# Performance work log

Hardware: AMD Instinct MI355X
Metric: run time of the kernel (lower is better)

Reference implementation:

```python
import jax, jax.numpy as jnp
import numpy as np

# Static config (matches init_kwargs)
N = 1024        # node_num
F = 64          # input_dim (window length)
D = 64          # dim == embed_dim (heads=1)
TOPK = 20
B = 64
EPS = 1e-5      # BatchNorm eps
NEG_SLOPE = 0.2 # GraphLayer leaky_relu slope


def setup_inputs() -> dict:
    key = jax.random.key(0)
    ks = jax.random.split(key, 12)
    s = lambda fan: 1.0 / np.sqrt(fan)
    inp = {
        'data': jax.random.normal(ks[0], (B, N, F), jnp.float32),
        'org_edge_index': jax.random.randint(ks[1], (2, 2048), 0, N),
        'embedding': jax.random.normal(ks[2], (N, D), jnp.float32) * s(D),   # nn.Embedding(node_num, dim), xavier-ish
        'lin_w': jax.random.normal(ks[3], (F, D), jnp.float32) * s(F),       # GraphLayer lin (bias=False)
        'att_i': jax.random.normal(ks[4], (D,), jnp.float32) * s(D),
        'att_j': jax.random.normal(ks[5], (D,), jnp.float32) * s(D),
        'att_em_i': jax.random.normal(ks[6], (D,), jnp.float32) * s(D),
        'att_em_j': jax.random.normal(ks[7], (D,), jnp.float32) * s(D),
        'gnn_bias': jnp.zeros((D,), jnp.float32),
        'bn1_gamma': jnp.ones((D,), jnp.float32),  # GNNLayer.bn
        'bn1_beta': jnp.zeros((D,), jnp.float32),
        'bn2_gamma': jnp.ones((D,), jnp.float32),  # bn_outlayer_in
        'bn2_beta': jnp.zeros((D,), jnp.float32),
        'out_w': jax.random.normal(ks[8], (D, 1), jnp.float32) * s(D),       # OutLayer Linear(dim, 1)
        'out_b': jnp.zeros((1,), jnp.float32),
    }
    return inp


def _batchnorm(x, gamma, beta, axes):
    # training-mode BatchNorm: batch statistics over `axes`, per-feature affine
    mu = jnp.mean(x, axis=axes, keepdims=True)
    var = jnp.var(x, axis=axes, keepdims=True)
    return gamma * (x - mu) * jax.lax.rsqrt(var + EPS) + beta


def reference(data, org_edge_index, embedding, lin_w, att_i, att_j, att_em_i,
              att_em_j, gnn_bias, bn1_gamma, bn1_beta, bn2_gamma, bn2_beta,
              out_w, out_b):
    # --- dynamic graph construction from embedding cosine similarity ---
    w = jax.lax.stop_gradient(embedding)          # weights_arr.detach()
    nrm = jnp.linalg.norm(w, axis=-1)
    cos = (w @ w.T) / jnp.clip(nrm[:, None] * nrm[None, :], 1e-10)
    _, topi = jax.lax.top_k(cos, TOPK)            # [N, TOPK] neighbors j of each target i
    # (torch code drops edges whose cos value is exactly 0 -- measure-zero with
    #  random embeddings; edge count stays N*TOPK. Self edge i->i is always in topk,
    #  matching remove_self_loops + add_self_loops.)

    # --- GraphLayer (GAT-style, heads=1, concat=False, aggr='add') ---
    xl = jnp.einsum('bnf,fd->bnd', data, lin_w)   # linear transform, [B,N,D]
    xj = xl[:, topi]                               # gather neighbor feats [B,N,TOPK,D]
    ej = embedding[topi]                           # neighbor embeddings [N,TOPK,D]
    # alpha = <key_i, att_i||att_em_i> + <key_j, att_j||att_em_j>
    score = (xl @ att_i)[:, :, None] \
          + (embedding @ att_em_i)[None, :, None] \
          + jnp.einsum('bnkd,d->bnk', xj, att_j) \
          + (ej @ att_em_j)[None]                  # [B,N,TOPK]
    alpha = jax.nn.softmax(jax.nn.leaky_relu(score, NEG_SLOPE), axis=-1)
    gnn = jnp.einsum('bnk,bnkd->bnd', alpha, xj) + gnn_bias

    # GNNLayer.bn: BatchNorm1d over B*N samples, D channels
    gnn = _batchnorm(gnn, bn1_gamma, bn1_beta, axes=(0, 1))

    # --- readout ---
    out = gnn * embedding[None]                    # mul with node embedding
    out = jax.nn.relu(_batchnorm(out, bn2_gamma, bn2_beta, axes=(0, 1)))
    # dropout(0.2) -> identity (eval)
    pred = (out @ out_w + out_b).reshape(B, N)     # OutLayer: Linear(D, 1)
    return pred, out
```

## Files before the change

### kernel.cpp

```cpp
#include <hip/hip_runtime.h>

#define NN 1024
#define KK 20
#define BN 65536
#define NEG_SLOPE 0.2f

typedef unsigned short u16;
typedef unsigned int u32;
typedef unsigned long long u64;
typedef __attribute__((ext_vector_type(8))) short bf8;
typedef __attribute__((ext_vector_type(4))) float f32x4;

__device__ __forceinline__ float bf2f(u16 h) {
    return __uint_as_float(((u32)h) << 16);
}
__device__ __forceinline__ u16 f2bf(float f) {
    u32 u = __float_as_uint(f);
    u32 lsb = (u >> 16) & 1u;
    u += 0x7fffu + lsb;
    return (u16)(u >> 16);
}
__device__ __forceinline__ void up2(u32 w, float& a, float& b) {
    a = __uint_as_float(w << 16);
    b = __uint_as_float(w & 0xffff0000u);
}
__device__ __forceinline__ bool is_bf(const void* g1) {
    return *(const u32*)g1 == 0x3F803F80u;
}
template <bool BF>
__device__ __forceinline__ float ldf(const void* p, size_t i) {
    if (BF) return bf2f(((const u16*)p)[i]);
    return ((const float*)p)[i];
}
template <bool BF>
__device__ __forceinline__ void stf(void* p, size_t i, float v) {
    if (BF) ((u16*)p)[i] = f2bf(v);
    else ((float*)p)[i] = v;
}
template <bool BF>
__device__ __forceinline__ void ldf2(const void* p, size_t pairidx, float& a, float& b) {
    if (BF) {
        u32 w = ((const u32*)p)[pairidx];
        up2(w, a, b);
    } else {
        float2 v = ((const float2*)p)[pairidx];
        a = v.x;
        b = v.y;
    }
}
__device__ __forceinline__ void gl2lds16(const void* g, void* l) {
    __builtin_amdgcn_global_load_lds(
        (const __attribute__((address_space(1))) u32*)g,
        (__attribute__((address_space(3))) u32*)l, 16, 0, 0);
}
__device__ __forceinline__ float ldstat(const float* p) {
    return __hip_atomic_load(p, __ATOMIC_RELAXED, __HIP_MEMORY_SCOPE_AGENT);
}

template <bool BF>
__device__ void k1a_body(const void* emb, const void* aei, const void* aej,
                         u16* nwH, u16* nwL, float* e_i, float* e_j, float* stats) {
    int tid = threadIdx.x;
    if (blockIdx.x == 0) {
        for (int s = tid; s < 464; s += 256) stats[s] = 0.f;
    }
    int lane = tid & 63, wave = tid >> 6;
    int n = blockIdx.x * 4 + wave;
    float v = ldf<BF>(emb, n * 64 + lane);
    float s2 = v * v;
    float si = v * ldf<BF>(aei, lane);
    float sj = v * ldf<BF>(aej, lane);
#pragma unroll
    for (int off = 32; off; off >>= 1) {
        s2 += __shfl_xor(s2, off, 64);
        si += __shfl_xor(si, off, 64);
        sj += __shfl_xor(sj, off, 64);
    }
    float rq = rsqrtf(fmaxf(s2, 1e-20f));
    float x = v * rq;
    u16 h = f2bf(x);
    nwH[n * 64 + lane] = h;
    nwL[n * 64 + lane] = f2bf(x - bf2f(h));
    if (lane == 0) { e_i[n] = si; e_j[n] = sj; }
}
__global__ __launch_bounds__(256) void k1a_norm(const void* emb, const void* aei, const void* aej,
                                                const void* probe, u16* nwH, u16* nwL,
                                                float* e_i, float* e_j, float* stats) {
    if (is_bf(probe)) k1a_body<true>(emb, aei, aej, nwH, nwL, e_i, e_j, stats);
    else k1a_body<false>(emb, aei, aej, nwH, nwL, e_i, e_j, stats);
}

__global__ __launch_bounds__(256) void k1b_gram(const u16* __restrict__ nwH,
                                                const u16* __restrict__ nwL,
                                                float* __restrict__ G) {
    int tid = threadIdx.x;
    int lane = tid & 63, wave = tid >> 6;
    int c = lane & 15, quad = lane >> 4;
    int rowblk = blockIdx.x >> 4, colblk = blockIdx.x & 15;
    int arow = rowblk * 64 + wave * 16 + c;
    bf8 aH[2], aL[2];
#pragma unroll
    for (int s = 0; s < 2; ++s) {
        aH[s] = *(const bf8*)(nwH + (size_t)arow * 64 + s * 32 + quad * 8);
        aL[s] = *(const bf8*)(nwL + (size_t)arow * 64 + s * 32 + quad * 8);
    }
    f32x4 acc[4] = {{0.f, 0.f, 0.f, 0.f}, {0.f, 0.f, 0.f, 0.f}, {0.f, 0.f, 0.f, 0.f}, {0.f, 0.f, 0.f, 0.f}};
#pragma unroll
    for (int t = 0; t < 4; ++t) {
        int bnode = colblk * 64 + t * 16 + c;
#pragma unroll
        for (int s = 0; s < 2; ++s) {
            bf8 bH = *(const bf8*)(nwH + (size_t)bnode * 64 + s * 32 + quad * 8);
            bf8 bL = *(const bf8*)(nwL + (size_t)bnode * 64 + s * 32 + quad * 8);
            acc[t] = __builtin_amdgcn_mfma_f32_16x16x32_bf16(aH[s], bH, acc[t], 0, 0, 0);
            acc[t] = __builtin_amdgcn_mfma_f32_16x16x32_bf16(aH[s], bL, acc[t], 0, 0, 0);
            acc[t] = __builtin_amdgcn_mfma_f32_16x16x32_bf16(aL[s], bH, acc[t], 0, 0, 0);
        }
    }
#pragma unroll
    for (int t = 0; t < 4; ++t) {
#pragma unroll
        for (int reg = 0; reg < 4; ++reg) {
            int row = rowblk * 64 + wave * 16 + quad * 4 + reg;
            G[(size_t)row * 1024 + colblk * 64 + t * 16 + c] = acc[t][reg];
        }
    }
}

__device__ void k1c_body(int blk, const float* __restrict__ G, int* __restrict__ topi) {
    int lane = threadIdx.x & 63, wave = threadIdx.x >> 6;
    int n = blk * 4 + wave;
    const f32x4* gp = (const f32x4*)(G + (size_t)n * 1024 + lane * 16);
    f32x4 v0 = gp[0], v1 = gp[1], v2 = gp[2], v3 = gp[3];
    float c[16] = {v0.x, v0.y, v0.z, v0.w, v1.x, v1.y, v1.z, v1.w,
                   v2.x, v2.y, v2.z, v2.w, v3.x, v3.y, v3.z, v3.w};
    u32 o[16];
#pragma unroll
    for (int j = 0; j < 16; ++j) {
        u32 u = __float_as_uint(c[j]);
        o[j] = u ^ (u32)(((int)u >> 31) | 0x80000000);
    }
    unsigned mask = 0u;
    int keep = 0;
    for (int r = 0; r < KK; ++r) {
        u32 bo = 0u;
        int bj = 0;
#pragma unroll
        for (int j = 0; j < 16; ++j) {
            bool t = !((mask >> j) & 1u) && o[j] > bo;
            bo = t ? o[j] : bo;
            bj = t ? j : bj;
        }
        u64 key = ((u64)bo << 32) | (u32)(~(u32)(lane * 16 + bj));
#pragma unroll
        for (int off = 32; off; off >>= 1) {
            u64 ok = __shfl_xor((unsigned long long)key, off, 64);
            key = ok > key ? ok : key;
        }
        int bm = (int)((~(u32)key) & 1023u);
        if ((bm >> 4) == lane) mask |= 1u << (bm & 15);
        if (lane == r) keep = bm;
    }
    if (lane < KK) topi[n * KK + lane] = keep;
}

template <bool BF>
__device__ void k2_body(int blk, const void* data, const void* lin_w, const void* att_i,
                        const void* att_j, u16* xl, float* a_i, float* a_j) {
    __shared__ u16 Bl[64 * 72];
    __shared__ u16 Ct[64 * 72];
    int tid = threadIdx.x;
    {
        int k = tid >> 2, n0 = (tid & 3) * 16;
        if (BF) {
            const u16* lw = (const u16*)lin_w;
#pragma unroll
            for (int i = 0; i < 16; ++i) Bl[(n0 + i) * 72 + k] = lw[k * 64 + n0 + i];
        } else {
            const float* lw = (const float*)lin_w;
#pragma unroll
            for (int i = 0; i < 16; ++i) Bl[(n0 + i) * 72 + k] = f2bf(lw[k * 64 + n0 + i]);
        }
    }
    __syncthreads();
    int lane = tid & 63, wave = tid >> 6;
    int c = lane & 15, quad = lane >> 4;
    int m0 = blk * 64 + wave * 16;
    size_t row = (size_t)(m0 + c);
    f32x4 acc[4] = {{0.f, 0.f, 0.f, 0.f}, {0.f, 0.f, 0.f, 0.f}, {0.f, 0.f, 0.f, 0.f}, {0.f, 0.f, 0.f, 0.f}};
#pragma unroll
    for (int s = 0; s < 2; ++s) {
        bf8 a;
        if (BF) {
            a = *(const bf8*)((const u16*)data + row * 64 + s * 32 + quad * 8);
        } else {
            const float* dp = (const float*)data + row * 64 + s * 32 + quad * 8;
            f32x4 x0 = *(const f32x4*)dp;
            f32x4 x1 = *(const f32x4*)(dp + 4);
            a[0] = (short)f2bf(x0.x); a[1] = (short)f2bf(x0.y);
            a[2] = (short)f2bf(x0.z); a[3] = (short)f2bf(x0.w);
            a[4] = (short)f2bf(x1.x); a[5] = (short)f2bf(x1.y);
            a[6] = (short)f2bf(x1.z); a[7] = (short)f2bf(x1.w);
        }
#pragma unroll
        for (int t = 0; t < 4; ++t) {
            bf8 b = *(const bf8*)&Bl[(t * 16 + c) * 72 + s * 32 + quad * 8];
            acc[t] = __builtin_amdgcn_mfma_f32_16x16x32_bf16(a, b, acc[t], 0, 0, 0);
        }
    }
    float wi[4], wj[4];
#pragma unroll
    for (int t = 0; t < 4; ++t) {
        wi[t] = ldf<BF>(att_i, t * 16 + c);
        wj[t] = ldf<BF>(att_j, t * 16 + c);
    }
    float ai4[4] = {0.f, 0.f, 0.f, 0.f}, aj4[4] = {0.f, 0.f, 0.f, 0.f};
#pragma unroll
    for (int t = 0; t < 4; ++t) {
#pragma unroll
        for (int reg = 0; reg < 4; ++reg) {
            float v = acc[t][reg];
            Ct[(wave * 16 + quad * 4 + reg) * 72 + t * 16 + c] = f2bf(v);
            ai4[reg] += v * wi[t];
            aj4[reg] += v * wj[t];
        }
    }
#pragma unroll
    for (int reg = 0; reg < 4; ++reg) {
#pragma unroll
        for (int off = 1; off < 16; off <<= 1) {
            ai4[reg] += __shfl_xor(ai4[reg], off, 64);
            aj4[reg] += __shfl_xor(aj4[reg], off, 64);
        }
    }
    if (c == 0) {
#pragma unroll
        for (int reg = 0; reg < 4; ++reg) {
            a_i[m0 + quad * 4 + reg] = ai4[reg];
            a_j[m0 + quad * 4 + reg] = aj4[reg];
        }
    }
    __syncthreads();
    {
        int r = tid >> 2, seg = tid & 3;
        uint4 v0 = *(const uint4*)&Ct[r * 72 + seg * 16];
        uint4 v1 = *(const uint4*)&Ct[r * 72 + seg * 16 + 8];
        uint4* dst = (uint4*)xl + ((size_t)(blk * 64 + r) * 8 + seg * 2);
        dst[0] = v0;
        dst[1] = v1;
    }
}

__global__ __launch_bounds__(256) void k12_fused(const void* data, const void* lin_w,
                                                 const void* att_i, const void* att_j,
                                                 const void* probe, u16* xl, float* a_i,
                                                 float* a_j, const float* G, int* topi) {
    if (blockIdx.x < 1024) {
        if (is_bf(probe)) k2_body<true>(blockIdx.x, data, lin_w, att_i, att_j, xl, a_i, a_j);
        else k2_body<false>(blockIdx.x, data, lin_w, att_i, att_j, xl, a_i, a_j);
    } else {
        k1c_body(blockIdx.x - 1024, G, topi);
    }
}

template <bool BF>
__device__ __forceinline__ void pqr_for(const float* stats, const void* g1, const void* b1,
                                        const void* g2, const void* b2, int d,
                                        float& P, float& Q, float& R) {
    double inv = 1.0 / 65536.0;
    double S1 = ldstat(stats + d), S2 = ldstat(stats + 64 + d);
    double T1 = ldstat(stats + 128 + d), T2 = ldstat(stats + 192 + d);
    double T3 = ldstat(stats + 256 + d), U1 = ldstat(stats + 320 + d), U2 = ldstat(stats + 384 + d);
    double mu1 = S1 * inv;
    double var1 = S2 * inv - mu1 * mu1;
    if (var1 < 0.0) var1 = 0.0;
    double r1 = 1.0 / sqrt(var1 + 1e-5);
    double A = (double)ldf<BF>(g1, d) * r1;
    double C = (double)ldf<BF>(b1, d) - A * mu1;
    double E1 = A * T1 + C * U1;
    double mu2 = E1 * inv;
    double E2 = A * A * T2 + 2.0 * A * C * T3 + C * C * U2;
    double var2 = E2 * inv - mu2 * mu2;
    if (var2 < 0.0) var2 = 0.0;
    double r2 = 1.0 / sqrt(var2 + 1e-5);
    double g2r2 = (double)ldf<BF>(g2, d) * r2;
    P = (float)(g2r2 * A);
    Q = (float)(g2r2 * C);
    R = (float)((double)ldf<BF>(b2, d) - g2r2 * mu2);
}
template <bool BF>
__device__ void k35_body(const u16* xl, const int* topi, const float* a_i, const float* a_j,
                         const float* e_i, const float* e_j, const void* emb,
                         const void* gnn_bias, const void* g1, const void* b1,
                         const void* g2, const void* b2, const void* out_w, const void* out_b,
                         float* stats, int* ctr, void* dout) {
    extern __shared__ char smem[];
    u32* slice = (u32*)smem;
    float* aje = (float*)(smem + 131072);
    float* aie = (float*)(smem + 135168);
    u32* sp = (u32*)(smem + 136192);
    int tid = threadIdx.x;
    int b = blockIdx.x & 63;
    int q = blockIdx.x >> 6;
    int n0 = q * 256;
    int lane = tid & 63, wave = tid >> 6;
    const char* srcb = (const char*)xl + (((size_t)b) << 17);
#pragma unroll
    for (int r = 0; r < 8; ++r) {
        int off = r * 16384 + wave * 1024;
        gl2lds16(srcb + off + lane * 16, (char*)smem + off);
    }
    aje[tid] = a_j[(b << 10) + tid] + e_j[tid];
    if (tid < 256) aie[tid] = a_i[(b << 10) + n0 + tid] + e_i[n0 + tid];
    __syncthreads();
    int half = lane >> 5, hl = lane & 31;
    int hwid = wave * 2 + half;
    int nl0 = hwid * 8;
#pragma unroll 2
    for (int ii = 0; ii < 8; ++ii) {
        int nl = nl0 + ii;
        int t = (hl < KK) ? topi[(n0 + nl) * KK + hl] : 0;
        float sc = -3e38f;
        if (hl < KK) {
            sc = aie[nl] + aje[t];
            sc = sc >= 0.f ? sc : NEG_SLOPE * sc;
        }
        float m = sc;
#pragma unroll
        for (int off = 16; off; off >>= 1) m = fmaxf(m, __shfl_xor(m, off, 32));
        float p = (hl < KK) ? __expf(sc - m) : 0.f;
        float S = p;
#pragma unroll
        for (int off = 16; off; off >>= 1) S += __shfl_xor(S, off, 32);
        if (hl < KK) sp[(hwid * 8 + ii) * KK + hl] = ((u32)f2bf(p / S) << 16) | (u32)t;
    }
    float bias0, bias1;
    ldf2<BF>(gnn_bias, hl, bias0, bias1);
    float se[14];
#pragma unroll
    for (int s = 0; s < 14; ++s) se[s] = 0.f;
    u32 gv[8];
#pragma unroll
    for (int ii = 0; ii < 8; ++ii) {
        int nl = nl0 + ii;
        int n = n0 + nl;
        const u32* spp = &sp[(hwid * 8 + ii) * KK];
        float a0e = 0.f, a0o = 0.f, a1e = 0.f, a1o = 0.f;
#pragma unroll
        for (int k = 0; k < KK; k += 2) {
            uint2 vv = *(const uint2*)&spp[k];
            u32 w0 = slice[((vv.x & 1023u) << 5) + hl];
            u32 w1 = slice[((vv.y & 1023u) << 5) + hl];
            float p0 = __uint_as_float(vv.x & 0xffff0000u);
            float p1 = __uint_as_float(vv.y & 0xffff0000u);
            a0e += p0 * __uint_as_float(w0 << 16);
            a1e += p0 * __uint_as_float(w0 & 0xffff0000u);
            a0o += p1 * __uint_as_float(w1 << 16);
            a1o += p1 * __uint_as_float(w1 & 0xffff0000u);
        }
        float acc0 = a0e + a0o + bias0;
        float acc1 = a1e + a1o + bias1;
        gv[ii] = (u32)f2bf(acc0) | ((u32)f2bf(acc1) << 16);
        float em0, em1;
        ldf2<BF>(emb, n * 32 + hl, em0, em1);
        se[0] += acc0; se[1] += acc1;
        se[2] += acc0 * acc0; se[3] += acc1 * acc1;
        float ge0 = acc0 * em0, ge1 = acc1 * em1;
        se[4] += ge0; se[5] += ge1;
        se[6] += ge0 * ge0; se[7] += ge1 * ge1;
        se[8] += ge0 * em0; se[9] += ge1 * em1;
        se[10] += em0; se[11] += em1;
        se[12] += em0 * em0; se[13] += em1 * em1;
    }
#pragma unroll
    for (int s = 0; s < 14; ++s) se[s] += __shfl_xor(se[s], 32, 64);
    __syncthreads();
    float* ps = (float*)smem;
    if (half == 0) {
#pragma unroll
        for (int s = 0; s < 7; ++s) {
            ps[wave * 448 + s * 64 + 2 * hl] = se[2 * s];
            ps[wave * 448 + s * 64 + 2 * hl + 1] = se[2 * s + 1];
        }
    }
    __syncthreads();
    if (tid < 448) {
        float s = 0.f;
#pragma unroll
        for (int w = 0; w < 16; ++w) s += ps[w * 448 + tid];
        atomicAdd(&stats[tid], s);
    }
    __syncthreads();
    if (tid == 0) {
        __hip_atomic_fetch_add(ctr, 1, __ATOMIC_ACQ_REL, __HIP_MEMORY_SCOPE_AGENT);
        while (__hip_atomic_load(ctr, __ATOMIC_ACQUIRE, __HIP_MEMORY_SCOPE_AGENT) < 256) {
            __builtin_amdgcn_s_sleep(8);
        }
    }
    __syncthreads();
    float P0, Q0, R0, P1, Q1, R1;
    pqr_for<BF>(stats, g1, b1, g2, b2, 2 * hl, P0, Q0, R0);
    pqr_for<BF>(stats, g1, b1, g2, b2, 2 * hl + 1, P1, Q1, R1);
    float wo0, wo1;
    ldf2<BF>(out_w, hl, wo0, wo1);
    float ob = ldf<BF>(out_b, 0);
#pragma unroll
    for (int ii = 0; ii < 8; ++ii) {
        int n = n0 + nl0 + ii;
        int pair = (b << 10) + n;
        float g0, g1v;
        up2(gv[ii], g0, g1v);
        float em0, em1;
        ldf2<BF>(emb, n * 32 + hl, em0, em1);
        float o0 = fmaxf(P0 * g0 * em0 + Q0 * em0 + R0, 0.f);
        float o1 = fmaxf(P1 * g1v * em1 + Q1 * em1 + R1, 0.f);
        if (BF) {
            ((u32*)dout)[(BN >> 1) + pair * 32 + hl] = (u32)f2bf(o0) | ((u32)f2bf(o1) << 16);
        } else {
            float2 v2; v2.x = o0; v2.y = o1;
            ((float2*)dout)[(BN >> 1) + pair * 32 + hl] = v2;
        }
        float p = o0 * wo0 + o1 * wo1;
#pragma unroll
        for (int off = 16; off; off >>= 1) p += __shfl_xor(p, off, 32);
        if (hl == 0) stf<BF>(dout, pair, p + ob);
    }
}
__global__ __launch_bounds__(1024) void k35_gnn(const u16* xl, const int* topi, const float* a_i,
                                                const float* a_j, const float* e_i, const float* e_j,
                                                const void* emb, const void* gnn_bias,
                                                const void* g1, const void* b1, const void* g2,
                                                const void* b2, const void* out_w, const void* out_b,
                                                float* stats, int* ctr, void* dout) {
    if (is_bf(g1)) k35_body<true>(xl, topi, a_i, a_j, e_i, e_j, emb, gnn_bias, g1, b1, g2, b2,
                                  out_w, out_b, stats, ctr, dout);
    else k35_body<false>(xl, topi, a_i, a_j, e_i, e_j, emb, gnn_bias, g1, b1, g2, b2,
                         out_w, out_b, stats, ctr, dout);
}

extern "C" void kernel_launch(void* const* d_in, const int* in_sizes, int n_in,
                              void* d_out, int out_size, void* d_ws, size_t ws_size,
                              hipStream_t stream) {
    const void* data = d_in[0];
    const void* emb = d_in[2];
    const void* lin_w = d_in[3];
    const void* att_i = d_in[4];
    const void* att_j = d_in[5];
    const void* att_em_i = d_in[6];
    const void* att_em_j = d_in[7];
    const void* gnn_bias = d_in[8];
    const void* bn1_g = d_in[9];
    const void* bn1_b = d_in[10];
    const void* bn2_g = d_in[11];
    const void* bn2_b = d_in[12];
    const void* out_w = d_in[13];
    const void* out_b = d_in[14];

    char* ws = (char*)d_ws;
    float* a_i = (float*)ws;
    float* a_j = a_i + 65536;
    float* e_i = a_j + 65536;
    float* e_j = e_i + 1024;
    float* stats = e_j + 1024;
    int* ctr = (int*)(stats + 448);
    int* topi = (int*)(stats + 464);
    u16* xl = (u16*)(topi + 20480);
    u16* nwH = xl + 4194304;
    u16* nwL = nwH + 65536;
    float* G = (float*)(nwL + 65536);

    k1a_norm<<<256, 256, 0, stream>>>(emb, att_em_i, att_em_j, bn1_g, nwH, nwL, e_i, e_j, stats);
    k1b_gram<<<256, 256, 0, stream>>>(nwH, nwL, G);
    k12_fused<<<1280, 256, 0, stream>>>(data, lin_w, att_i, att_j, bn1_g, xl, a_i, a_j, G, topi);
    k35_gnn<<<256, 1024, 156672, stream>>>(xl, topi, a_i, a_j, e_i, e_j, emb, gnn_bias,
                                           bn1_g, bn1_b, bn2_g, bn2_b, out_w, out_b,
                                           stats, ctr, d_out);
}
```

Measured before the change: 157.3 us.

## Gather neighbor features from global memory and split GNN kernel into smaller blocks

```diff
diff --git a/kernel.cpp b/kernel.cpp
--- a/kernel.cpp
+++ b/kernel.cpp
@@ -48,11 +48,6 @@
         b = v.y;
     }
 }
-__device__ __forceinline__ void gl2lds16(const void* g, void* l) {
-    __builtin_amdgcn_global_load_lds(
-        (const __attribute__((address_space(1))) u32*)g,
-        (__attribute__((address_space(3))) u32*)l, 16, 0, 0);
-}
 __device__ __forceinline__ float ldstat(const float* p) {
     return __hip_atomic_load(p, __ATOMIC_RELAXED, __HIP_MEMORY_SCOPE_AGENT);
 }
@@ -62,7 +57,7 @@
                          u16* nwH, u16* nwL, float* e_i, float* e_j, float* stats) {
     int tid = threadIdx.x;
     if (blockIdx.x == 0) {
-        for (int s = tid; s < 464; s += 256) stats[s] = 0.f;
+        for (int s = tid; s < 1808; s += 256) stats[s] = 0.f;
     }
     int lane = tid & 63, wave = tid >> 6;
     int n = blockIdx.x * 4 + wave;
@@ -264,13 +259,15 @@
 }
 
 template <bool BF>
-__device__ __forceinline__ void pqr_for(const float* stats, const void* g1, const void* b1,
+__device__ __forceinline__ void pqr_lds(const float* sc, const void* g1, const void* b1,
                                         const void* g2, const void* b2, int d,
                                         float& P, float& Q, float& R) {
     double inv = 1.0 / 65536.0;
-    double S1 = ldstat(stats + d), S2 = ldstat(stats + 64 + d);
-    double T1 = ldstat(stats + 128 + d), T2 = ldstat(stats + 192 + d);
-    double T3 = ldstat(stats + 256 + d), U1 = ldstat(stats + 320 + d), U2 = ldstat(stats + 384 + d);
+#define SUM4(off) ((double)sc[(off) + d] + (double)sc[448 + (off) + d] + \
+                   (double)sc[896 + (off) + d] + (double)sc[1344 + (off) + d])
+    double S1 = SUM4(0), S2 = SUM4(64), T1 = SUM4(128), T2 = SUM4(192);
+    double T3 = SUM4(256), U1 = SUM4(320), U2 = SUM4(384);
+#undef SUM4
     double mu1 = S1 * inv;
     double var1 = S2 * inv - mu1 * mu1;
     if (var1 < 0.0) var1 = 0.0;
@@ -289,33 +286,28 @@
     R = (float)((double)ldf<BF>(b2, d) - g2r2 * mu2);
 }
 template <bool BF>
-__device__ void k35_body(const u16* xl, const int* topi, const float* a_i, const float* a_j,
+__device__ void k3g_body(const u16* xl, const int* topi, const float* a_i, const float* a_j,
                          const float* e_i, const float* e_j, const void* emb,
                          const void* gnn_bias, const void* g1, const void* b1,
                          const void* g2, const void* b2, const void* out_w, const void* out_b,
                          float* stats, int* ctr, void* dout) {
-    extern __shared__ char smem[];
-    u32* slice = (u32*)smem;
-    float* aje = (float*)(smem + 131072);
-    float* aie = (float*)(smem + 135168);
-    u32* sp = (u32*)(smem + 136192);
+    __shared__ float aje[1024];
+    __shared__ float aie[128];
+    __shared__ u32 sp[16 * 8 * KK];
+    __shared__ float ps[8 * 448];
     int tid = threadIdx.x;
-    int b = blockIdx.x & 63;
-    int q = blockIdx.x >> 6;
-    int n0 = q * 256;
+    int bid = blockIdx.x;
+    int b = bid & 63;
+    int j = bid >> 6;
+    int n0 = j * 128;
     int lane = tid & 63, wave = tid >> 6;
-    const char* srcb = (const char*)xl + (((size_t)b) << 17);
-#pragma unroll
-    for (int r = 0; r < 8; ++r) {
-        int off = r * 16384 + wave * 1024;
-        gl2lds16(srcb + off + lane * 16, (char*)smem + off);
-    }
-    aje[tid] = a_j[(b << 10) + tid] + e_j[tid];
-    if (tid < 256) aie[tid] = a_i[(b << 10) + n0 + tid] + e_i[n0 + tid];
-    __syncthreads();
     int half = lane >> 5, hl = lane & 31;
     int hwid = wave * 2 + half;
     int nl0 = hwid * 8;
+    aje[tid] = a_j[(b << 10) + tid] + e_j[tid];
+    aje[tid + 512] = a_j[(b << 10) + tid + 512] + e_j[tid + 512];
+    if (tid < 128) aie[tid] = a_i[(b << 10) + n0 + tid] + e_i[n0 + tid];
+    __syncthreads();
 #pragma unroll 2
     for (int ii = 0; ii < 8; ++ii) {
         int nl = nl0 + ii;
@@ -340,6 +332,8 @@
 #pragma unroll
     for (int s = 0; s < 14; ++s) se[s] = 0.f;
     u32 gv[8];
+    const u32* __restrict__ xg = (const u32*)xl + ((size_t)b << 15);
+    __syncthreads();
 #pragma unroll
     for (int ii = 0; ii < 8; ++ii) {
         int nl = nl0 + ii;
@@ -349,8 +343,8 @@
 #pragma unroll
         for (int k = 0; k < KK; k += 2) {
             uint2 vv = *(const uint2*)&spp[k];
-            u32 w0 = slice[((vv.x & 1023u) << 5) + hl];
-            u32 w1 = slice[((vv.y & 1023u) << 5) + hl];
+            u32 w0 = xg[((vv.x & 1023u) << 5) + hl];
+            u32 w1 = xg[((vv.y & 1023u) << 5) + hl];
             float p0 = __uint_as_float(vv.x & 0xffff0000u);
             float p1 = __uint_as_float(vv.y & 0xffff0000u);
             a0e += p0 * __uint_as_float(w0 << 16);
@@ -375,7 +369,6 @@
 #pragma unroll
     for (int s = 0; s < 14; ++s) se[s] += __shfl_xor(se[s], 32, 64);
     __syncthreads();
-    float* ps = (float*)smem;
     if (half == 0) {
 #pragma unroll
         for (int s = 0; s < 7; ++s) {
@@ -387,20 +380,22 @@
     if (tid < 448) {
         float s = 0.f;
 #pragma unroll
-        for (int w = 0; w < 16; ++w) s += ps[w * 448 + tid];
-        atomicAdd(&stats[tid], s);
+        for (int w = 0; w < 8; ++w) s += ps[w * 448 + tid];
+        atomicAdd(&stats[(b & 3) * 448 + tid], s);
     }
     __syncthreads();
     if (tid == 0) {
         __hip_atomic_fetch_add(ctr, 1, __ATOMIC_ACQ_REL, __HIP_MEMORY_SCOPE_AGENT);
-        while (__hip_atomic_load(ctr, __ATOMIC_ACQUIRE, __HIP_MEMORY_SCOPE_AGENT) < 256) {
+        while (__hip_atomic_load(ctr, __ATOMIC_ACQUIRE, __HIP_MEMORY_SCOPE_AGENT) < 512) {
             __builtin_amdgcn_s_sleep(8);
         }
     }
     __syncthreads();
+    for (int s = tid; s < 1792; s += 512) ps[s] = ldstat(stats + s);
+    __syncthreads();
     float P0, Q0, R0, P1, Q1, R1;
-    pqr_for<BF>(stats, g1, b1, g2, b2, 2 * hl, P0, Q0, R0);
-    pqr_for<BF>(stats, g1, b1, g2, b2, 2 * hl + 1, P1, Q1, R1);
+    pqr_lds<BF>(ps, g1, b1, g2, b2, 2 * hl, P0, Q0, R0);
+    pqr_lds<BF>(ps, g1, b1, g2, b2, 2 * hl + 1, P1, Q1, R1);
     float wo0, wo1;
     ldf2<BF>(out_w, hl, wo0, wo1);
     float ob = ldf<BF>(out_b, 0);
@@ -426,15 +421,15 @@
         if (hl == 0) stf<BF>(dout, pair, p + ob);
     }
 }
-__global__ __launch_bounds__(1024) void k35_gnn(const u16* xl, const int* topi, const float* a_i,
-                                                const float* a_j, const float* e_i, const float* e_j,
-                                                const void* emb, const void* gnn_bias,
-                                                const void* g1, const void* b1, const void* g2,
-                                                const void* b2, const void* out_w, const void* out_b,
-                                                float* stats, int* ctr, void* dout) {
-    if (is_bf(g1)) k35_body<true>(xl, topi, a_i, a_j, e_i, e_j, emb, gnn_bias, g1, b1, g2, b2,
+__global__ __launch_bounds__(512, 4) void k3g_gnn(const u16* xl, const int* topi, const float* a_i,
+                                                  const float* a_j, const float* e_i, const float* e_j,
+                                                  const void* emb, const void* gnn_bias,
+                                                  const void* g1, const void* b1, const void* g2,
+                                                  const void* b2, const void* out_w, const void* out_b,
+                                                  float* stats, int* ctr, void* dout) {
+    if (is_bf(g1)) k3g_body<true>(xl, topi, a_i, a_j, e_i, e_j, emb, gnn_bias, g1, b1, g2, b2,
                                   out_w, out_b, stats, ctr, dout);
-    else k35_body<false>(xl, topi, a_i, a_j, e_i, e_j, emb, gnn_bias, g1, b1, g2, b2,
+    else k3g_body<false>(xl, topi, a_i, a_j, e_i, e_j, emb, gnn_bias, g1, b1, g2, b2,
                          out_w, out_b, stats, ctr, dout);
 }
 
@@ -462,8 +457,8 @@
     float* e_i = a_j + 65536;
     float* e_j = e_i + 1024;
     float* stats = e_j + 1024;
-    int* ctr = (int*)(stats + 448);
-    int* topi = (int*)(stats + 464);
+    int* ctr = (int*)(stats + 1792);
+    int* topi = (int*)(stats + 1808);
     u16* xl = (u16*)(topi + 20480);
     u16* nwH = xl + 4194304;
     u16* nwL = nwH + 65536;
@@ -472,7 +467,7 @@
     k1a_norm<<<256, 256, 0, stream>>>(emb, att_em_i, att_em_j, bn1_g, nwH, nwL, e_i, e_j, stats);
     k1b_gram<<<256, 256, 0, stream>>>(nwH, nwL, G);
     k12_fused<<<1280, 256, 0, stream>>>(data, lin_w, att_i, att_j, bn1_g, xl, a_i, a_j, G, topi);
-    k35_gnn<<<256, 1024, 156672, stream>>>(xl, topi, a_i, a_j, e_i, e_j, emb, gnn_bias,
-                                           bn1_g, bn1_b, bn2_g, bn2_b, out_w, out_b,
-                                           stats, ctr, d_out);
-}
+    k3g_gnn<<<512, 512, 0, stream>>>(xl, topi, a_i, a_j, e_i, e_j, emb, gnn_bias,
+                                     bn1_g, bn1_b, bn2_g, bn2_b, out_w, out_b,
+                                     stats, ctr, d_out);
+}
```

New measurement: 207.5 us. 1.32x slower.

## Remap GNN kernel to 16-lane groups with 4 features per lane

Applied to the files above, without the earlier changes.

```diff
diff --git a/kernel.cpp b/kernel.cpp
--- a/kernel.cpp
+++ b/kernel.cpp
@@ -47,11 +47,6 @@
         a = v.x;
         b = v.y;
     }
-}
-__device__ __forceinline__ void gl2lds16(const void* g, void* l) {
-    __builtin_amdgcn_global_load_lds(
-        (const __attribute__((address_space(1))) u32*)g,
-        (__attribute__((address_space(3))) u32*)l, 16, 0, 0);
 }
 __device__ __forceinline__ float ldstat(const float* p) {
     return __hip_atomic_load(p, __ATOMIC_RELAXED, __HIP_MEMORY_SCOPE_AGENT);
@@ -264,13 +259,12 @@
 }
 
 template <bool BF>
-__device__ __forceinline__ void pqr_for(const float* stats, const void* g1, const void* b1,
+__device__ __forceinline__ void pqr_lds(const float* sc, const void* g1, const void* b1,
                                         const void* g2, const void* b2, int d,
                                         float& P, float& Q, float& R) {
     double inv = 1.0 / 65536.0;
-    double S1 = ldstat(stats + d), S2 = ldstat(stats + 64 + d);
-    double T1 = ldstat(stats + 128 + d), T2 = ldstat(stats + 192 + d);
-    double T3 = ldstat(stats + 256 + d), U1 = ldstat(stats + 320 + d), U2 = ldstat(stats + 384 + d);
+    double S1 = sc[d], S2 = sc[64 + d], T1 = sc[128 + d], T2 = sc[192 + d];
+    double T3 = sc[256 + d], U1 = sc[320 + d], U2 = sc[384 + d];
     double mu1 = S1 * inv;
     double var1 = S2 * inv - mu1 * mu1;
     if (var1 < 0.0) var1 = 0.0;
@@ -289,98 +283,111 @@
     R = (float)((double)ldf<BF>(b2, d) - g2r2 * mu2);
 }
 template <bool BF>
-__device__ void k35_body(const u16* xl, const int* topi, const float* a_i, const float* a_j,
-                         const float* e_i, const float* e_j, const void* emb,
-                         const void* gnn_bias, const void* g1, const void* b1,
-                         const void* g2, const void* b2, const void* out_w, const void* out_b,
-                         float* stats, int* ctr, void* dout) {
+__device__ void k35b_body(const u16* xl, const int* topi, const float* a_i, const float* a_j,
+                          const float* e_i, const float* e_j, const void* emb,
+                          const void* gnn_bias, const void* g1, const void* b1,
+                          const void* g2, const void* b2, const void* out_w, const void* out_b,
+                          float* stats, int* ctr, void* dout) {
     extern __shared__ char smem[];
     u32* slice = (u32*)smem;
     float* aje = (float*)(smem + 131072);
     float* aie = (float*)(smem + 135168);
-    u32* sp = (u32*)(smem + 136192);
+    u32* spg = (u32*)(smem + 136192);
     int tid = threadIdx.x;
     int b = blockIdx.x & 63;
     int q = blockIdx.x >> 6;
     int n0 = q * 256;
     int lane = tid & 63, wave = tid >> 6;
-    const char* srcb = (const char*)xl + (((size_t)b) << 17);
-#pragma unroll
-    for (int r = 0; r < 8; ++r) {
-        int off = r * 16384 + wave * 1024;
-        gl2lds16(srcb + off + lane * 16, (char*)smem + off);
-    }
+    const uint4* src = (const uint4*)(xl + ((size_t)b << 16));
+    uint4* dst = (uint4*)slice;
+#pragma unroll
+    for (int r = 0; r < 8; ++r) dst[r * 1024 + tid] = src[r * 1024 + tid];
     aje[tid] = a_j[(b << 10) + tid] + e_j[tid];
     if (tid < 256) aie[tid] = a_i[(b << 10) + n0 + tid] + e_i[n0 + tid];
     __syncthreads();
-    int half = lane >> 5, hl = lane & 31;
-    int hwid = wave * 2 + half;
-    int nl0 = hwid * 8;
+    int gid = tid >> 4, glane = tid & 15;
+    u32* spp = &spg[gid * 24];
+    float bias0, bias1, bias2, bias3;
+    ldf2<BF>(gnn_bias, 2 * glane, bias0, bias1);
+    ldf2<BF>(gnn_bias, 2 * glane + 1, bias2, bias3);
+    float se[28];
+#pragma unroll
+    for (int s = 0; s < 28; ++s) se[s] = 0.f;
+    u32 gvw[8];
 #pragma unroll 2
-    for (int ii = 0; ii < 8; ++ii) {
-        int nl = nl0 + ii;
-        int t = (hl < KK) ? topi[(n0 + nl) * KK + hl] : 0;
-        float sc = -3e38f;
-        if (hl < KK) {
-            sc = aie[nl] + aje[t];
-            sc = sc >= 0.f ? sc : NEG_SLOPE * sc;
-        }
-        float m = sc;
-#pragma unroll
-        for (int off = 16; off; off >>= 1) m = fmaxf(m, __shfl_xor(m, off, 32));
-        float p = (hl < KK) ? __expf(sc - m) : 0.f;
-        float S = p;
-#pragma unroll
-        for (int off = 16; off; off >>= 1) S += __shfl_xor(S, off, 32);
-        if (hl < KK) sp[(hwid * 8 + ii) * KK + hl] = ((u32)f2bf(p / S) << 16) | (u32)t;
-    }
-    float bias0, bias1;
-    ldf2<BF>(gnn_bias, hl, bias0, bias1);
-    float se[14];
-#pragma unroll
-    for (int s = 0; s < 14; ++s) se[s] = 0.f;
-    u32 gv[8];
-#pragma unroll
-    for (int ii = 0; ii < 8; ++ii) {
-        int nl = nl0 + ii;
+    for (int ii = 0; ii < 4; ++ii) {
+        int nl = gid * 4 + ii;
         int n = n0 + nl;
-        const u32* spp = &sp[(hwid * 8 + ii) * KK];
-        float a0e = 0.f, a0o = 0.f, a1e = 0.f, a1o = 0.f;
+        int ta = topi[n * KK + glane];
+        float aien = aie[nl];
+        float sa = aien + aje[ta];
+        sa = sa >= 0.f ? sa : NEG_SLOPE * sa;
+        int tb = 0;
+        float sb = -3e38f;
+        if (glane < 4) {
+            tb = topi[n * KK + 16 + glane];
+            sb = aien + aje[tb];
+            sb = sb >= 0.f ? sb : NEG_SLOPE * sb;
+        }
+        float m = fmaxf(sa, sb);
+#pragma unroll
+        for (int off = 8; off; off >>= 1) m = fmaxf(m, __shfl_xor(m, off, 64));
+        float pa = __expf(sa - m);
+        float pb = (glane < 4) ? __expf(sb - m) : 0.f;
+        float S = pa + pb;
+#pragma unroll
+        for (int off = 8; off; off >>= 1) S += __shfl_xor(S, off, 64);
+        spp[glane] = ((u32)f2bf(pa / S) << 16) | (u32)ta;
+        if (glane < 4) spp[16 + glane] = ((u32)f2bf(pb / S) << 16) | (u32)tb;
+        float a0e = 0.f, a1e = 0.f, a2e = 0.f, a3e = 0.f;
+        float a0o = 0.f, a1o = 0.f, a2o = 0.f, a3o = 0.f;
 #pragma unroll
         for (int k = 0; k < KK; k += 2) {
             uint2 vv = *(const uint2*)&spp[k];
-            u32 w0 = slice[((vv.x & 1023u) << 5) + hl];
-            u32 w1 = slice[((vv.y & 1023u) << 5) + hl];
+            uint2 w0 = *(const uint2*)&slice[(vv.x & 1023u) * 32 + 2 * glane];
+            uint2 w1 = *(const uint2*)&slice[(vv.y & 1023u) * 32 + 2 * glane];
             float p0 = __uint_as_float(vv.x & 0xffff0000u);
             float p1 = __uint_as_float(vv.y & 0xffff0000u);
-            a0e += p0 * __uint_as_float(w0 << 16);
-            a1e += p0 * __uint_as_float(w0 & 0xffff0000u);
-            a0o += p1 * __uint_as_float(w1 << 16);
-            a1o += p1 * __uint_as_float(w1 & 0xffff0000u);
+            a0e += p0 * __uint_as_float(w0.x << 16);
+            a1e += p0 * __uint_as_float(w0.x & 0xffff0000u);
+            a2e += p0 * __uint_as_float(w0.y << 16);
+            a3e += p0 * __uint_as_float(w0.y & 0xffff0000u);
+            a0o += p1 * __uint_as_float(w1.x << 16);
+            a1o += p1 * __uint_as_float(w1.x & 0xffff0000u);
+            a2o += p1 * __uint_as_float(w1.y << 16);
+            a3o += p1 * __uint_as_float(w1.y & 0xffff0000u);
         }
         float acc0 = a0e + a0o + bias0;
         float acc1 = a1e + a1o + bias1;
-        gv[ii] = (u32)f2bf(acc0) | ((u32)f2bf(acc1) << 16);
-        float em0, em1;
-        ldf2<BF>(emb, n * 32 + hl, em0, em1);
-        se[0] += acc0; se[1] += acc1;
-        se[2] += acc0 * acc0; se[3] += acc1 * acc1;
-        float ge0 = acc0 * em0, ge1 = acc1 * em1;
-        se[4] += ge0; se[5] += ge1;
-        se[6] += ge0 * ge0; se[7] += ge1 * ge1;
-        se[8] += ge0 * em0; se[9] += ge1 * em1;
-        se[10] += em0; se[11] += em1;
-        se[12] += em0 * em0; se[13] += em1 * em1;
-    }
-#pragma unroll
-    for (int s = 0; s < 14; ++s) se[s] += __shfl_xor(se[s], 32, 64);
+        float acc2 = a2e + a2o + bias2;
+        float acc3 = a3e + a3o + bias3;
+        gvw[2 * ii] = (u32)f2bf(acc0) | ((u32)f2bf(acc1) << 16);
+        gvw[2 * ii + 1] = (u32)f2bf(acc2) | ((u32)f2bf(acc3) << 16);
+        float em0, em1, em2, em3;
+        ldf2<BF>(emb, n * 32 + 2 * glane, em0, em1);
+        ldf2<BF>(emb, n * 32 + 2 * glane + 1, em2, em3);
+        float ge0 = acc0 * em0, ge1 = acc1 * em1, ge2 = acc2 * em2, ge3 = acc3 * em3;
+        se[0] += acc0; se[1] += acc1; se[2] += acc2; se[3] += acc3;
+        se[4] += acc0 * acc0; se[5] += acc1 * acc1; se[6] += acc2 * acc2; se[7] += acc3 * acc3;
+        se[8] += ge0; se[9] += ge1; se[10] += ge2; se[11] += ge3;
+        se[12] += ge0 * ge0; se[13] += ge1 * ge1; se[14] += ge2 * ge2; se[15] += ge3 * ge3;
+        se[16] += ge0 * em0; se[17] += ge1 * em1; se[18] += ge2 * em2; se[19] += ge3 * em3;
+        se[20] += em0; se[21] += em1; se[22] += em2; se[23] += em3;
+        se[24] += em0 * em0; se[25] += em1 * em1; se[26] += em2 * em2; se[27] += em3 * em3;
+    }
+#pragma unroll
+    for (int s = 0; s < 28; ++s) {
+        se[s] += __shfl_xor(se[s], 16, 64);
+        se[s] += __shfl_xor(se[s], 32, 64);
+    }
     __syncthreads();
     float* ps = (float*)smem;
-    if (half == 0) {
+    if (lane < 16) {
 #pragma unroll
         for (int s = 0; s < 7; ++s) {
-            ps[wave * 448 + s * 64 + 2 * hl] = se[2 * s];
-            ps[wave * 448 + s * 64 + 2 * hl + 1] = se[2 * s + 1];
+#pragma unroll
+            for (int c = 0; c < 4; ++c)
+                ps[wave * 448 + s * 64 + 4 * glane + c] = se[s * 4 + c];
         }
     }
     __syncthreads();
@@ -398,44 +405,60 @@
         }
     }
     __syncthreads();
-    float P0, Q0, R0, P1, Q1, R1;
-    pqr_for<BF>(stats, g1, b1, g2, b2, 2 * hl, P0, Q0, R0);
-    pqr_for<BF>(stats, g1, b1, g2, b2, 2 * hl + 1, P1, Q1, R1);
-    float wo0, wo1;
-    ldf2<BF>(out_w, hl, wo0, wo1);
+    float* sc = aje;
+    if (tid < 448) sc[tid] = ldstat(stats + tid);
+    __syncthreads();
+    float P0, Q0, R0, P1, Q1, R1, P2, Q2, R2, P3, Q3, R3;
+    pqr_lds<BF>(sc, g1, b1, g2, b2, 4 * glane, P0, Q0, R0);
+    pqr_lds<BF>(sc, g1, b1, g2, b2, 4 * glane + 1, P1, Q1, R1);
+    pqr_lds<BF>(sc, g1, b1, g2, b2, 4 * glane + 2, P2, Q2, R2);
+    pqr_lds<BF>(sc, g1, b1, g2, b2, 4 * glane + 3, P3, Q3, R3);
+    float wo0, wo1, wo2, wo3;
+    ldf2<BF>(out_w, 2 * glane, wo0, wo1);
+    ldf2<BF>(out_w, 2 * glane + 1, wo2, wo3);
     float ob = ldf<BF>(out_b, 0);
 #pragma unroll
-    for (int ii = 0; ii < 8; ++ii) {
-        int n = n0 + nl0 + ii;
+    for (int ii = 0; ii < 4; ++ii) {
+        int n = n0 + gid * 4 + ii;
         int pair = (b << 10) + n;
-        float g0, g1v;
-        up2(gv[ii], g0, g1v);
-        float em0, em1;
-        ldf2<BF>(emb, n * 32 + hl, em0, em1);
-        float o0 = fmaxf(P0 * g0 * em0 + Q0 * em0 + R0, 0.f);
-        float o1 = fmaxf(P1 * g1v * em1 + Q1 * em1 + R1, 0.f);
+        float v0, v1, v2, v3;
+        up2(gvw[2 * ii], v0, v1);
+        up2(gvw[2 * ii + 1], v2, v3);
+        float em0, em1, em2, em3;
+        ldf2<BF>(emb, n * 32 + 2 * glane, em0, em1);
+        ldf2<BF>(emb, n * 32 + 2 * glane + 1, em2, em3);
+        float o0 = fmaxf(P0 * v0 * em0 + Q0 * em0 + R0, 0.f);
+        float o1 = fmaxf(P1 * v1 * em1 + Q1 * em1 + R1, 0.f);
+        float o2 = fmaxf(P2 * v2 * em2 + Q2 * em2 + R2, 0.f);
+        float o3 = fmaxf(P3 * v3 * em3 + Q3 * em3 + R3, 0.f);
         if (BF) {
-            ((u32*)dout)[(BN >> 1) + pair * 32 + hl] = (u32)f2bf(o0) | ((u32)f2bf(o1) << 16);
+            uint2 ov;
+            ov.x = (u32)f2bf(o0) | ((u32)f2bf(o1) << 16);
+            ov.y = (u32)f2bf(o2) | ((u32)f2bf(o3) << 16);
+            *(uint2*)&((u32*)dout)[(BN >> 1) + pair * 32 + 2 * glane] = ov;
         } else {
-            float2 v2; v2.x = o0; v2.y = o1;
-            ((float2*)dout)[(BN >> 1) + pair * 32 + hl] = v2;
-        }
-        float p = o0 * wo0 + o1 * wo1;
-#pragma unroll
-        for (int off = 16; off; off >>= 1) p += __shfl_xor(p, off, 32);
-        if (hl == 0) stf<BF>(dout, pair, p + ob);
-    }
-}
-__global__ __launch_bounds__(1024) void k35_gnn(const u16* xl, const int* topi, const float* a_i,
-                                                const float* a_j, const float* e_i, const float* e_j,
-                                                const void* emb, const void* gnn_bias,
-                                                const void* g1, const void* b1, const void* g2,
-                                                const void* b2, const void* out_w, const void* out_b,
-                                                float* stats, int* ctr, void* dout) {
-    if (is_bf(g1)) k35_body<true>(xl, topi, a_i, a_j, e_i, e_j, emb, gnn_bias, g1, b1, g2, b2,
-                                  out_w, out_b, stats, ctr, dout);
-    else k35_body<false>(xl, topi, a_i, a_j, e_i, e_j, emb, gnn_bias, g1, b1, g2, b2,
-                         out_w, out_b, stats, ctr, dout);
+            float4 ov;
+            ov.x = o0; ov.y = o1; ov.z = o2; ov.w = o3;
+            ((float4*)dout)[(BN >> 2) + pair * 16 + glane] = ov;
+        }
+        float p = o0 * wo0 + o1 * wo1 + o2 * wo2 + o3 * wo3;
+#pragma unroll
+        for (int off = 8; off; off >>= 1) p += __shfl_xor(p, off, 64);
+        if (glane == 0) stf<BF>(dout, pair, p + ob);
+    }
+}
+__global__ __launch_bounds__(1024, 4) void k35b_gnn(const u16* xl, const int* topi,
+                                                    const float* a_i, const float* a_j,
+                                                    const float* e_i, const float* e_j,
+                                                    const void* emb, const void* gnn_bias,
+                                                    const void* g1, const void* b1, const void* g2,
+                                                    const void* b2, const void* out_w,
+                                                    const void* out_b, float* stats, int* ctr,
+                                                    void* dout) {
+    if (is_bf(g1)) k35b_body<true>(xl, topi, a_i, a_j, e_i, e_j, emb, gnn_bias, g1, b1, g2, b2,
+                                   out_w, out_b, stats, ctr, dout);
+    else k35b_body<false>(xl, topi, a_i, a_j, e_i, e_j, emb, gnn_bias, g1, b1, g2, b2,
+                          out_w, out_b, stats, ctr, dout);
 }
 
 extern "C" void kernel_launch(void* const* d_in, const int* in_sizes, int n_in,
@@ -472,7 +495,7 @@
     k1a_norm<<<256, 256, 0, stream>>>(emb, att_em_i, att_em_j, bn1_g, nwH, nwL, e_i, e_j, stats);
     k1b_gram<<<256, 256, 0, stream>>>(nwH, nwL, G);
     k12_fused<<<1280, 256, 0, stream>>>(data, lin_w, att_i, att_j, bn1_g, xl, a_i, a_j, G, topi);
-    k35_gnn<<<256, 1024, 156672, stream>>>(xl, topi, a_i, a_j, e_i, e_j, emb, gnn_bias,
-                                           bn1_g, bn1_b, bn2_g, bn2_b, out_w, out_b,
-                                           stats, ctr, d_out);
-}
+    k35b_gnn<<<256, 1024, 142336, stream>>>(xl, topi, a_i, a_j, e_i, e_j, emb, gnn_bias,
+                                            bn1_g, bn1_b, bn2_g, bn2_b, out_w, out_b,
+                                            stats, ctr, d_out);
+}
```

Result: no change. 154.8 us (-1.6%).
